# Kernel optimization log

Hardware: AMD Instinct MI355X
Metric: run time of the kernel (lower is better)

## Reference

```python
import jax, jax.numpy as jnp
import numpy as np

N = 100000      # nodes
E = 1600000     # edges (avg degree 16)
NF = 1          # node_feature_dim
EF = 1          # edge_feature_dim
H = 64          # hidden_dim
L = 5           # num_layers


def _linear_init(key, fan_in, fan_out):
    # torch nn.Linear default: U(-1/sqrt(fan_in), 1/sqrt(fan_in)) for W and b
    s = 1.0 / np.sqrt(fan_in)
    kw, kb = jax.random.split(key)
    w = jax.random.uniform(kw, (fan_in, fan_out), minval=-s, maxval=s, dtype=jnp.float32)
    b = jax.random.uniform(kb, (fan_out,), minval=-s, maxval=s, dtype=jnp.float32)
    return w, b


def setup_inputs() -> dict:
    key = jax.random.key(0)
    ks = jax.random.split(key, 8)
    x = jax.random.normal(ks[0], (N, NF), dtype=jnp.float32)
    edge_index = jax.random.randint(ks[1], (2, E), 0, N, dtype=jnp.int32)
    edge_attr = jax.random.uniform(ks[2], (E, EF), dtype=jnp.float32)

    emb_w, emb_b = _linear_init(ks[3], NF, H)
    fc_w, fc_b = _linear_init(ks[4], H, 1)

    msg_w1, msg_b1, msg_w2, msg_b2 = [], [], [], []
    upd_w1, upd_b1, upd_w2, upd_b2 = [], [], [], []
    lk = jax.random.split(ks[5], L)
    for l in range(L):
        k1, k2, k3, k4 = jax.random.split(lk[l], 4)
        w, b = _linear_init(k1, H + EF, H); msg_w1.append(w); msg_b1.append(b)
        w, b = _linear_init(k2, H, H);      msg_w2.append(w); msg_b2.append(b)
        w, b = _linear_init(k3, 2 * H, H);  upd_w1.append(w); upd_b1.append(b)
        w, b = _linear_init(k4, H, H);      upd_w2.append(w); upd_b2.append(b)

    stack = lambda xs: jnp.stack(xs, axis=0)
    return {
        "x": x, "edge_index": edge_index, "edge_attr": edge_attr,
        "emb_w": emb_w, "emb_b": emb_b,
        "msg_w1": stack(msg_w1), "msg_b1": stack(msg_b1),
        "msg_w2": stack(msg_w2), "msg_b2": stack(msg_b2),
        "upd_w1": stack(upd_w1), "upd_b1": stack(upd_b1),
        "upd_w2": stack(upd_w2), "upd_b2": stack(upd_b2),
        "fc_w": fc_w, "fc_b": fc_b,
    }


def reference(x, edge_index, edge_attr, emb_w, emb_b,
              msg_w1, msg_b1, msg_w2, msg_b2,
              upd_w1, upd_b1, upd_w2, upd_b2, fc_w, fc_b):
    src = edge_index[0]  # x_j (source)
    dst = edge_index[1]  # aggregation target i
    n = x.shape[0]

    h = x @ emb_w + emb_b  # [N, H]
    for l in range(msg_w1.shape[0]):
        # message: MLP(cat[x_j, edge_attr])
        m = jnp.concatenate([h[src], edge_attr], axis=1)  # [E, H+EF]
        m = jax.nn.relu(m @ msg_w1[l] + msg_b1[l]) @ msg_w2[l] + msg_b2[l]  # [E, H]
        # scatter-min aggregate; torch_scatter fills empty segments with 0
        aggr = jax.ops.segment_min(m, dst, num_segments=n)
        aggr = jnp.where(jnp.isfinite(aggr), aggr, jnp.zeros_like(aggr))
        # update: MLP(cat[x, aggr])
        u = jnp.concatenate([h, aggr], axis=1)  # [N, 2H]
        h = jax.nn.relu(u @ upd_w1[l] + upd_b1[l]) @ upd_w2[l] + upd_b2[l]
    return (h @ fc_w + fc_b).squeeze(-1)  # [N]
```

## Files before the change

### kernel.cpp

```cpp
#include <hip/hip_runtime.h>
#include <math.h>

#define N_NODES 100000
#define N_EDGES 1600000
#define HDIM 64
#define SCAN_T 1024
#define SCAN_CHUNK 98
#define NPB 128
#define LBLOCKS 782

__device__ __forceinline__ unsigned encMin(float f) {
  unsigned u = __float_as_uint(f);
  return (u & 0x80000000u) ? ~u : (u | 0x80000000u);
}
__device__ __forceinline__ float decMin(unsigned u) {
  unsigned b = (u & 0x80000000u) ? (u & 0x7FFFFFFFu) : ~u;
  return __uint_as_float(b);
}


__global__ __launch_bounds__(256) void k_zero_int(int* __restrict__ p, int n) {
  int i = blockIdx.x * 256 + threadIdx.x;
  if (i < n) p[i] = 0;
}

__global__ __launch_bounds__(256) void k_deg_count(const int* __restrict__ ei,
                                                   int* __restrict__ deg) {
  int e = blockIdx.x * 256 + threadIdx.x;
  if (e < N_EDGES) atomicAdd(&deg[ei[N_EDGES + e]], 1);
}

__global__ __launch_bounds__(SCAN_T) void k_rowptr(const int* __restrict__ deg,
                                                   int* __restrict__ row_ptr) {
  __shared__ int sums[SCAN_T];
  const int t = threadIdx.x;
  const int lo = t * SCAN_CHUNK;
  const int hi = min(lo + SCAN_CHUNK, N_NODES);
  int s = 0;
  for (int i = lo; i < hi; ++i) s += deg[i];
  sums[t] = s;
  __syncthreads();
  for (int off = 1; off < SCAN_T; off <<= 1) {
    int v = (t >= off) ? sums[t - off] : 0;
    __syncthreads();
    sums[t] += v;
    __syncthreads();
  }
  int run = (t == 0) ? 0 : sums[t - 1];
  for (int i = lo; i < hi; ++i) { row_ptr[i] = run; run += deg[i]; }
  if (t == SCAN_T - 1) row_ptr[N_NODES] = run;
}

__global__ __launch_bounds__(256) void k_scatter(
    const int* __restrict__ ei, const float* __restrict__ eattr,
    const int* __restrict__ row_ptr, int* __restrict__ cursor,
    int* __restrict__ s_src, float* __restrict__ s_ea, int* __restrict__ s_dl) {
  int e = blockIdx.x * 256 + threadIdx.x;
  if (e >= N_EDGES) return;
  int d = ei[N_EDGES + e];
  int pos = row_ptr[d] + atomicAdd(&cursor[d], 1);
  s_src[pos] = ei[e];
  s_ea[pos] = eattr[e];
  s_dl[pos] = d & (NPB - 1);
}


__global__ __launch_bounds__(256) void k_embed_z(
    const float* __restrict__ x, const float* __restrict__ emb_w,
    const float* __restrict__ emb_b,
    const float* __restrict__ w1, const float* __restrict__ b1,
    float* __restrict__ h, float* __restrict__ z) {
  __shared__ float hs[64][65];
  const int t = threadIdx.x;
  const int nl = t >> 2;
  const int l4 = t & 3;
  const int i = blockIdx.x * 64 + nl;
  const bool valid = (i < N_NODES);
  const int jbase = l4 * 16;
  const float xv = valid ? x[i] : 0.0f;

  float hv[16];
  #pragma unroll
  for (int jj = 0; jj < 16; ++jj) {
    int j = jbase + jj;
    hv[jj] = fmaf(xv, emb_w[j], emb_b[j]);
    hs[nl][j] = hv[jj];
  }
  if (valid) {
    #pragma unroll
    for (int q = 0; q < 4; ++q)
      reinterpret_cast<float4*>(h + (size_t)i * HDIM)[l4 * 4 + q] =
          make_float4(hv[4*q], hv[4*q+1], hv[4*q+2], hv[4*q+3]);
  }
  __syncthreads();

  float acc[16];
  #pragma unroll
  for (int jj = 0; jj < 16; ++jj) acc[jj] = b1[jbase + jj];
  #pragma unroll 8
  for (int k = 0; k < 64; ++k) {
    float hk = hs[nl][k];
    const float* wr = w1 + k * 64 + jbase;
    #pragma unroll
    for (int jj = 0; jj < 16; ++jj) acc[jj] = fmaf(hk, wr[jj], acc[jj]);
  }
  if (valid) {
    #pragma unroll
    for (int q = 0; q < 4; ++q)
      reinterpret_cast<float4*>(z + (size_t)i * HDIM)[l4 * 4 + q] =
          make_float4(acc[4*q], acc[4*q+1], acc[4*q+2], acc[4*q+3]);
  }
}

template <int LAST>
__global__ __launch_bounds__(256) void k_layer(
    const int* __restrict__ row_ptr,
    const int* __restrict__ s_src, const float* __restrict__ s_ea,
    const int* __restrict__ s_dl,
    const float* __restrict__ z_in,
    const float* __restrict__ w1b, const float* __restrict__ w2,
    const float* __restrict__ b2,
    const float* __restrict__ u1w, const float* __restrict__ u1b,
    const float* __restrict__ u2w, const float* __restrict__ u2b,
    const float* __restrict__ w1next, const float* __restrict__ b1next,
    const float* __restrict__ fcw, const float* __restrict__ fcb,
    float* __restrict__ h, float* __restrict__ z_out, float* __restrict__ out) {
  __shared__ float hid_s[4][8][68];
  __shared__ unsigned acc_u[NPB][65];
  __shared__ float ps[NPB][2];
  float* acc_f = (float*)acc_u;

  const int t = threadIdx.x;
  const int lane = t & 63;
  const int w = __builtin_amdgcn_readfirstlane(t >> 6);
  const int nbase = blockIdx.x * NPB;

  for (int i = t; i < NPB * 65; i += 256) ((unsigned*)acc_u)[i] = 0xFFFFFFFFu;
  __syncthreads();

  {
    const int eb0 = row_ptr[nbase];
    const int eb1 = row_ptr[min(nbase + NPB, N_NODES)];
    const int n = eb1 - eb0;
    const int we0 = eb0 + (n * w) / 4;
    const int we1 = eb0 + (n * (w + 1)) / 4;

    const int eL = lane >> 3;
    const int q  = lane & 7;
    const float4 w1bA = ((const float4*)w1b)[q];
    const float4 w1bB = ((const float4*)w1b)[8 + q];
    const float b2c = b2[lane];
    float w2c[64];
    #pragma unroll
    for (int k = 0; k < 64; ++k) w2c[k] = w2[k * 64 + lane];

    float run = INFINITY;
    int cur = -1;

    float4 ra, rb; float eaR = 0.0f;
    ra = make_float4(0.f,0.f,0.f,0.f); rb = ra;
    if (we0 + eL < we1) {
      const int src = s_src[we0 + eL];
      const float4* zr = (const float4*)(z_in + (size_t)src * HDIM);
      ra = zr[q]; rb = zr[8 + q];
      eaR = s_ea[we0 + eL];
    }

    for (int b = we0; b < we1; b += 8) {
      float4 na = make_float4(0.f,0.f,0.f,0.f), nb = na; float ean = 0.0f;
      if (b + 8 + eL < we1) {
        const int srcn = s_src[b + 8 + eL];
        const float4* zrn = (const float4*)(z_in + (size_t)srcn * HDIM);
        na = zrn[q]; nb = zrn[8 + q];
        ean = s_ea[b + 8 + eL];
      }
      if (b + eL < we1) {
        float4 h0, h1;
        h0.x = fmaxf(fmaf(eaR, w1bA.x, ra.x), 0.f);
        h0.y = fmaxf(fmaf(eaR, w1bA.y, ra.y), 0.f);
        h0.z = fmaxf(fmaf(eaR, w1bA.z, ra.z), 0.f);
        h0.w = fmaxf(fmaf(eaR, w1bA.w, ra.w), 0.f);
        h1.x = fmaxf(fmaf(eaR, w1bB.x, rb.x), 0.f);
        h1.y = fmaxf(fmaf(eaR, w1bB.y, rb.y), 0.f);
        h1.z = fmaxf(fmaf(eaR, w1bB.z, rb.z), 0.f);
        h1.w = fmaxf(fmaf(eaR, w1bB.w, rb.w), 0.f);
        *(float4*)&hid_s[w][eL][q * 4] = h0;
        *(float4*)&hid_s[w][eL][32 + q * 4] = h1;
      }
      #pragma unroll
      for (int e2 = 0; e2 < 8; ++e2) {
        if (b + e2 >= we1) break;
        float m0 = b2c, m1 = 0.f, m2 = 0.f, m3 = 0.f;
        #pragma unroll
        for (int k4 = 0; k4 < 16; ++k4) {
          float4 hq = *(const float4*)&hid_s[w][e2][k4 * 4];
          m0 = fmaf(hq.x, w2c[4*k4+0], m0);
          m1 = fmaf(hq.y, w2c[4*k4+1], m1);
          m2 = fmaf(hq.z, w2c[4*k4+2], m2);
          m3 = fmaf(hq.w, w2c[4*k4+3], m3);
        }
        float m = (m0 + m1) + (m2 + m3);
        const int dl = s_dl[b + e2];
        if (dl != cur) {
          if (cur >= 0) atomicMin(&acc_u[cur][lane], encMin(run));
          cur = dl; run = INFINITY;
        }
        run = fminf(run, m);
      }
      ra = na; rb = nb; eaR = ean;
    }
    if (cur >= 0) atomicMin(&acc_u[cur][lane], encMin(run));
  }
  __syncthreads();

  const int half = w & 1;
  const int pr = w >> 1;
  const int jb = half * 32;
  const int nl = pr * 64 + lane;
  const int node = nbase + nl;
  const bool valid = (node < N_NODES);
  const size_t off = (size_t)(valid ? node : 0) * HDIM;

  #pragma unroll
  for (int j = 0; j < 32; ++j) {
    float f = decMin(acc_u[nl][jb + j]);
    if (!isfinite(f)) f = 0.f;
    acc_f[nl * 65 + jb + j] = f;
  }
  __syncthreads();

  float acc[32];
  #pragma unroll
  for (int j = 0; j < 32; ++j) acc[j] = u1b[jb + j];
  {
    const float4* hr = reinterpret_cast<const float4*>(h + off);
    for (int k4 = 0; k4 < 16; ++k4) {
      float4 uv = hr[k4];
      const float* w0 = u1w + (4*k4+0) * 64 + jb;
      const float* w1 = u1w + (4*k4+1) * 64 + jb;
      const float* w2r = u1w + (4*k4+2) * 64 + jb;
      const float* w3 = u1w + (4*k4+3) * 64 + jb;
      #pragma unroll
      for (int j = 0; j < 32; ++j) acc[j] = fmaf(uv.x, w0[j], acc[j]);
      #pragma unroll
      for (int j = 0; j < 32; ++j) acc[j] = fmaf(uv.y, w1[j], acc[j]);
      #pragma unroll
      for (int j = 0; j < 32; ++j) acc[j] = fmaf(uv.z, w2r[j], acc[j]);
      #pragma unroll
      for (int j = 0; j < 32; ++j) acc[j] = fmaf(uv.w, w3[j], acc[j]);
    }
    #pragma unroll 4
    for (int k = 0; k < 64; ++k) {
      float uk = acc_f[nl * 65 + k];
      const float* wr = u1w + (64 + k) * 64 + jb;
      #pragma unroll
      for (int j = 0; j < 32; ++j) acc[j] = fmaf(uk, wr[j], acc[j]);
    }
  }
  __syncthreads();
  #pragma unroll
  for (int j = 0; j < 32; ++j) acc_f[nl * 65 + jb + j] = fmaxf(acc[j], 0.f);
  __syncthreads();

  float hn[32];
  #pragma unroll
  for (int j = 0; j < 32; ++j) hn[j] = u2b[jb + j];
  #pragma unroll 4
  for (int k = 0; k < 64; ++k) {
    float hk = acc_f[nl * 65 + k];
    const float* wr = u2w + k * 64 + jb;
    #pragma unroll
    for (int j = 0; j < 32; ++j) hn[j] = fmaf(hk, wr[j], hn[j]);
  }
  if (valid) {
    #pragma unroll
    for (int v = 0; v < 8; ++v)
      reinterpret_cast<float4*>(h + off)[half * 8 + v] =
          make_float4(hn[4*v], hn[4*v+1], hn[4*v+2], hn[4*v+3]);
  }

  if (LAST) {
    float s = 0.0f;
    #pragma unroll
    for (int j = 0; j < 32; ++j) s = fmaf(hn[j], fcw[jb + j], s);
    ps[nl][half] = s;
    __syncthreads();
    if (half == 0 && valid) out[node] = ps[nl][0] + ps[nl][1] + fcb[0];
  } else {
    __syncthreads();
    #pragma unroll
    for (int j = 0; j < 32; ++j) acc_f[nl * 65 + jb + j] = hn[j];
    __syncthreads();
    float zz[32];
    #pragma unroll
    for (int j = 0; j < 32; ++j) zz[j] = b1next[jb + j];
    #pragma unroll 4
    for (int k = 0; k < 64; ++k) {
      float hk = acc_f[nl * 65 + k];
      const float* wr = w1next + k * 64 + jb;
      #pragma unroll
      for (int j = 0; j < 32; ++j) zz[j] = fmaf(hk, wr[j], zz[j]);
    }
    if (valid) {
      #pragma unroll
      for (int v = 0; v < 8; ++v)
        reinterpret_cast<float4*>(z_out + off)[half * 8 + v] =
            make_float4(zz[4*v], zz[4*v+1], zz[4*v+2], zz[4*v+3]);
    }
  }
}

extern "C" void kernel_launch(void* const* d_in, const int* in_sizes, int n_in,
                              void* d_out, int out_size, void* d_ws, size_t ws_size,
                              hipStream_t stream) {
  const float* x      = (const float*)d_in[0];
  const int*   ei     = (const int*)d_in[1];
  const float* eattr  = (const float*)d_in[2];
  const float* emb_w  = (const float*)d_in[3];
  const float* emb_b  = (const float*)d_in[4];
  const float* msg_w1 = (const float*)d_in[5];
  const float* msg_b1 = (const float*)d_in[6];
  const float* msg_w2 = (const float*)d_in[7];
  const float* msg_b2 = (const float*)d_in[8];
  const float* upd_w1 = (const float*)d_in[9];
  const float* upd_b1 = (const float*)d_in[10];
  const float* upd_w2 = (const float*)d_in[11];
  const float* upd_b2 = (const float*)d_in[12];
  const float* fc_w   = (const float*)d_in[13];
  const float* fc_b   = (const float*)d_in[14];
  float* out = (float*)d_out;

  float* h     = (float*)d_ws;
  float* zA    = h + (size_t)N_NODES * HDIM;
  float* zB    = zA + (size_t)N_NODES * HDIM;
  float* s_ea  = zB + (size_t)N_NODES * HDIM;
  int*   s_src = (int*)(s_ea + N_EDGES);
  int*   s_dl  = s_src + N_EDGES;
  int*   row_ptr = s_dl + N_EDGES;
  int*   deg   = row_ptr + (N_NODES + 1);
  int*   cursor= deg + N_NODES;

  const int nodeBlocks64 = (N_NODES + 63) / 64;
  const int edgeBlocks = (N_EDGES + 255) / 256;

  k_zero_int<<<(2 * N_NODES + 255) / 256, 256, 0, stream>>>(deg, 2 * N_NODES);
  k_deg_count<<<edgeBlocks, 256, 0, stream>>>(ei, deg);
  k_rowptr<<<1, SCAN_T, 0, stream>>>(deg, row_ptr);
  k_scatter<<<edgeBlocks, 256, 0, stream>>>(ei, eattr, row_ptr, cursor,
                                            s_src, s_ea, s_dl);

  k_embed_z<<<nodeBlocks64, 256, 0, stream>>>(x, emb_w, emb_b, msg_w1, msg_b1, h, zA);

  float* zin = zA;
  float* zout = zB;
  for (int l = 0; l < 5; ++l) {
    const float* w1b = msg_w1 + l * 65 * 64 + 64 * 64;
    const float* w2  = msg_w2 + l * 64 * 64;
    const float* b2  = msg_b2 + l * 64;
    const float* u1w = upd_w1 + l * 128 * 64;
    const float* u1b = upd_b1 + l * 64;
    const float* u2w = upd_w2 + l * 64 * 64;
    const float* u2b = upd_b2 + l * 64;
    if (l < 4) {
      k_layer<0><<<LBLOCKS, 256, 0, stream>>>(
          row_ptr, s_src, s_ea, s_dl, zin,
          w1b, w2, b2, u1w, u1b, u2w, u2b,
          msg_w1 + (l + 1) * 65 * 64, msg_b1 + (l + 1) * 64,
          nullptr, nullptr,
          h, zout, nullptr);
      float* tmp = zin; zin = zout; zout = tmp;
    } else {
      k_layer<1><<<LBLOCKS, 256, 0, stream>>>(
          row_ptr, s_src, s_ea, s_dl, zin,
          w1b, w2, b2, u1w, u1b, u2w, u2b,
          nullptr, nullptr,
          fc_w, fc_b,
          h, nullptr, out);
    }
  }
}
```

Before: 2.560 ms.

## Restructure edge message MLP into batched 64-edge tiles with edge-per-lane matmul

Edge processing now works in 64-edge batches per wave pair. Each batch writes the hidden activations to shared memory, then each lane computes one edge's 32 output channels, with the w2 weights read as wave-uniform scalars instead of held as a 64-register column per lane. The per-node update MLP also drops to 64 nodes per block, with each wave computing 16 output columns, which doubles the block count. In exchange there are several block-wide barriers per batch, an extra shared-memory round trip for the message outputs, and the old prefetch of the next edge's gather is gone.

```diff
diff --git a/kernel.cpp b/kernel.cpp
--- a/kernel.cpp
+++ b/kernel.cpp
@@ -6,8 +6,9 @@
 #define HDIM 64
 #define SCAN_T 1024
 #define SCAN_CHUNK 98
-#define NPB 128
-#define LBLOCKS 782
+#define NPB 64
+#define LBLOCKS 1563
+#define BSTRIDE 66
 
 __device__ __forceinline__ unsigned encMin(float f) {
   unsigned u = __float_as_uint(f);
@@ -125,187 +126,204 @@
     const float* __restrict__ w1next, const float* __restrict__ b1next,
     const float* __restrict__ fcw, const float* __restrict__ fcb,
     float* __restrict__ h, float* __restrict__ z_out, float* __restrict__ out) {
-  __shared__ float hid_s[4][8][68];
+  __shared__ float buf[2][64][BSTRIDE];
   __shared__ unsigned acc_u[NPB][65];
-  __shared__ float ps[NPB][2];
+  __shared__ float ps[NPB][4];
   float* acc_f = (float*)acc_u;
 
   const int t = threadIdx.x;
   const int lane = t & 63;
   const int w = __builtin_amdgcn_readfirstlane(t >> 6);
+  const int pair = w >> 1;
+  const int wi = w & 1;
   const int nbase = blockIdx.x * NPB;
 
   for (int i = t; i < NPB * 65; i += 256) ((unsigned*)acc_u)[i] = 0xFFFFFFFFu;
-  __syncthreads();
-
-  {
-    const int eb0 = row_ptr[nbase];
-    const int eb1 = row_ptr[min(nbase + NPB, N_NODES)];
-    const int n = eb1 - eb0;
-    const int we0 = eb0 + (n * w) / 4;
-    const int we1 = eb0 + (n * (w + 1)) / 4;
-
-    const int eL = lane >> 3;
-    const int q  = lane & 7;
-    const float4 w1bA = ((const float4*)w1b)[q];
-    const float4 w1bB = ((const float4*)w1b)[8 + q];
-    const float b2c = b2[lane];
-    float w2c[64];
-    #pragma unroll
-    for (int k = 0; k < 64; ++k) w2c[k] = w2[k * 64 + lane];
-
-    float run = INFINITY;
-    int cur = -1;
-
-    float4 ra, rb; float eaR = 0.0f;
-    ra = make_float4(0.f,0.f,0.f,0.f); rb = ra;
-    if (we0 + eL < we1) {
-      const int src = s_src[we0 + eL];
-      const float4* zr = (const float4*)(z_in + (size_t)src * HDIM);
-      ra = zr[q]; rb = zr[8 + q];
-      eaR = s_ea[we0 + eL];
-    }
-
-    for (int b = we0; b < we1; b += 8) {
-      float4 na = make_float4(0.f,0.f,0.f,0.f), nb = na; float ean = 0.0f;
-      if (b + 8 + eL < we1) {
-        const int srcn = s_src[b + 8 + eL];
-        const float4* zrn = (const float4*)(z_in + (size_t)srcn * HDIM);
-        na = zrn[q]; nb = zrn[8 + q];
-        ean = s_ea[b + 8 + eL];
+
+  const int eb0 = row_ptr[nbase];
+  const int eb1 = row_ptr[min(nbase + NPB, N_NODES)];
+  const int n = eb1 - eb0;
+  const int emid = eb0 + (n >> 1);
+  const int p0 = pair ? emid : eb0;
+  const int p1 = pair ? eb1 : emid;
+  const int nbat = ((n - (n >> 1)) + 63) >> 6;
+
+  const int rq = lane >> 3;
+  const int q  = lane & 7;
+  const float4 w1bA = ((const float4*)w1b)[q];
+  const float4 w1bB = ((const float4*)w1b)[q + 8];
+  const int jb = wi * 32;
+
+  __syncthreads();
+
+  for (int bi = 0; bi < nbat; ++bi) {
+    const int base = p0 + (bi << 6);
+    const int cnt  = min(64, p1 - base);
+
+    if (cnt > 0) {
+      #pragma unroll
+      for (int i = 0; i < 4; ++i) {
+        const int row = wi * 32 + i * 8 + rq;
+        const int ed = base + row;
+        const bool v = (row < cnt);
+        const int src = v ? s_src[ed] : 0;
+        const float ea = v ? s_ea[ed] : 0.0f;
+        const float4* zr = (const float4*)(z_in + (size_t)src * HDIM);
+        float4 a = zr[q];
+        float4 b = zr[q + 8];
+        float2 h0, h1, h2, h3;
+        h0.x = fmaxf(fmaf(ea, w1bA.x, a.x), 0.f);
+        h0.y = fmaxf(fmaf(ea, w1bA.y, a.y), 0.f);
+        h1.x = fmaxf(fmaf(ea, w1bA.z, a.z), 0.f);
+        h1.y = fmaxf(fmaf(ea, w1bA.w, a.w), 0.f);
+        h2.x = fmaxf(fmaf(ea, w1bB.x, b.x), 0.f);
+        h2.y = fmaxf(fmaf(ea, w1bB.y, b.y), 0.f);
+        h3.x = fmaxf(fmaf(ea, w1bB.z, b.z), 0.f);
+        h3.y = fmaxf(fmaf(ea, w1bB.w, b.w), 0.f);
+        float* bp = &buf[pair][row][0];
+        *(float2*)&bp[q * 4]          = h0;
+        *(float2*)&bp[q * 4 + 2]      = h1;
+        *(float2*)&bp[32 + q * 4]     = h2;
+        *(float2*)&bp[32 + q * 4 + 2] = h3;
       }
-      if (b + eL < we1) {
-        float4 h0, h1;
-        h0.x = fmaxf(fmaf(eaR, w1bA.x, ra.x), 0.f);
-        h0.y = fmaxf(fmaf(eaR, w1bA.y, ra.y), 0.f);
-        h0.z = fmaxf(fmaf(eaR, w1bA.z, ra.z), 0.f);
-        h0.w = fmaxf(fmaf(eaR, w1bA.w, ra.w), 0.f);
-        h1.x = fmaxf(fmaf(eaR, w1bB.x, rb.x), 0.f);
-        h1.y = fmaxf(fmaf(eaR, w1bB.y, rb.y), 0.f);
-        h1.z = fmaxf(fmaf(eaR, w1bB.z, rb.z), 0.f);
-        h1.w = fmaxf(fmaf(eaR, w1bB.w, rb.w), 0.f);
-        *(float4*)&hid_s[w][eL][q * 4] = h0;
-        *(float4*)&hid_s[w][eL][32 + q * 4] = h1;
+    }
+    __syncthreads();
+
+    float m[32];
+    if (cnt > 0) {
+      #pragma unroll
+      for (int c = 0; c < 32; ++c) m[c] = b2[jb + c];
+      const float* bp = &buf[pair][lane][0];
+      #pragma unroll 4
+      for (int k2 = 0; k2 < 32; ++k2) {
+        float2 hq = *(const float2*)&bp[k2 * 2];
+        const float* wr0 = w2 + (2 * k2 + 0) * 64 + jb;
+        const float* wr1 = w2 + (2 * k2 + 1) * 64 + jb;
+        #pragma unroll
+        for (int c = 0; c < 32; ++c) m[c] = fmaf(hq.x, wr0[c], m[c]);
+        #pragma unroll
+        for (int c = 0; c < 32; ++c) m[c] = fmaf(hq.y, wr1[c], m[c]);
       }
-      #pragma unroll
-      for (int e2 = 0; e2 < 8; ++e2) {
-        if (b + e2 >= we1) break;
-        float m0 = b2c, m1 = 0.f, m2 = 0.f, m3 = 0.f;
-        #pragma unroll
-        for (int k4 = 0; k4 < 16; ++k4) {
-          float4 hq = *(const float4*)&hid_s[w][e2][k4 * 4];
-          m0 = fmaf(hq.x, w2c[4*k4+0], m0);
-          m1 = fmaf(hq.y, w2c[4*k4+1], m1);
-          m2 = fmaf(hq.z, w2c[4*k4+2], m2);
-          m3 = fmaf(hq.w, w2c[4*k4+3], m3);
-        }
-        float m = (m0 + m1) + (m2 + m3);
-        const int dl = s_dl[b + e2];
+    }
+    __syncthreads();
+
+    if (cnt > 0) {
+      float* bp = &buf[pair][lane][jb];
+      #pragma unroll
+      for (int c2 = 0; c2 < 16; ++c2)
+        *(float2*)&bp[c2 * 2] = make_float2(m[2*c2], m[2*c2+1]);
+    }
+    __syncthreads();
+
+    if (cnt > 0) {
+      const int e0 = wi * 32;
+      const int e1 = min(wi * 32 + 32, cnt);
+      float run = INFINITY;
+      int cur = -1;
+      for (int e = e0; e < e1; ++e) {
+        const int dl = s_dl[base + e];
         if (dl != cur) {
           if (cur >= 0) atomicMin(&acc_u[cur][lane], encMin(run));
           cur = dl; run = INFINITY;
         }
-        run = fminf(run, m);
+        run = fminf(run, buf[pair][e][lane]);
       }
-      ra = na; rb = nb; eaR = ean;
-    }
-    if (cur >= 0) atomicMin(&acc_u[cur][lane], encMin(run));
-  }
-  __syncthreads();
-
-  const int half = w & 1;
-  const int pr = w >> 1;
-  const int jb = half * 32;
-  const int nl = pr * 64 + lane;
-  const int node = nbase + nl;
+      if (cur >= 0) atomicMin(&acc_u[cur][lane], encMin(run));
+    }
+    __syncthreads();
+  }
+
+  const int jq = w * 16;
+  const int node = nbase + lane;
   const bool valid = (node < N_NODES);
   const size_t off = (size_t)(valid ? node : 0) * HDIM;
 
   #pragma unroll
-  for (int j = 0; j < 32; ++j) {
-    float f = decMin(acc_u[nl][jb + j]);
+  for (int j = 0; j < 16; ++j) {
+    float f = decMin(acc_u[lane][jq + j]);
     if (!isfinite(f)) f = 0.f;
-    acc_f[nl * 65 + jb + j] = f;
-  }
-  __syncthreads();
-
-  float acc[32];
-  #pragma unroll
-  for (int j = 0; j < 32; ++j) acc[j] = u1b[jb + j];
+    acc_f[lane * 65 + jq + j] = f;
+  }
+  __syncthreads();
+
+  float acc[16];
+  #pragma unroll
+  for (int j = 0; j < 16; ++j) acc[j] = u1b[jq + j];
   {
     const float4* hr = reinterpret_cast<const float4*>(h + off);
     for (int k4 = 0; k4 < 16; ++k4) {
       float4 uv = hr[k4];
-      const float* w0 = u1w + (4*k4+0) * 64 + jb;
-      const float* w1 = u1w + (4*k4+1) * 64 + jb;
-      const float* w2r = u1w + (4*k4+2) * 64 + jb;
-      const float* w3 = u1w + (4*k4+3) * 64 + jb;
-      #pragma unroll
-      for (int j = 0; j < 32; ++j) acc[j] = fmaf(uv.x, w0[j], acc[j]);
-      #pragma unroll
-      for (int j = 0; j < 32; ++j) acc[j] = fmaf(uv.y, w1[j], acc[j]);
-      #pragma unroll
-      for (int j = 0; j < 32; ++j) acc[j] = fmaf(uv.z, w2r[j], acc[j]);
-      #pragma unroll
-      for (int j = 0; j < 32; ++j) acc[j] = fmaf(uv.w, w3[j], acc[j]);
+      const float* w0 = u1w + (4*k4+0) * 64 + jq;
+      const float* w1 = u1w + (4*k4+1) * 64 + jq;
+      const float* w2r = u1w + (4*k4+2) * 64 + jq;
+      const float* w3 = u1w + (4*k4+3) * 64 + jq;
+      #pragma unroll
+      for (int j = 0; j < 16; ++j) acc[j] = fmaf(uv.x, w0[j], acc[j]);
+      #pragma unroll
+      for (int j = 0; j < 16; ++j) acc[j] = fmaf(uv.y, w1[j], acc[j]);
+      #pragma unroll
+      for (int j = 0; j < 16; ++j) acc[j] = fmaf(uv.z, w2r[j], acc[j]);
+      #pragma unroll
+      for (int j = 0; j < 16; ++j) acc[j] = fmaf(uv.w, w3[j], acc[j]);
     }
     #pragma unroll 4
     for (int k = 0; k < 64; ++k) {
-      float uk = acc_f[nl * 65 + k];
-      const float* wr = u1w + (64 + k) * 64 + jb;
-      #pragma unroll
-      for (int j = 0; j < 32; ++j) acc[j] = fmaf(uk, wr[j], acc[j]);
-    }
-  }
-  __syncthreads();
-  #pragma unroll
-  for (int j = 0; j < 32; ++j) acc_f[nl * 65 + jb + j] = fmaxf(acc[j], 0.f);
-  __syncthreads();
-
-  float hn[32];
-  #pragma unroll
-  for (int j = 0; j < 32; ++j) hn[j] = u2b[jb + j];
+      float uk = acc_f[lane * 65 + k];
+      const float* wr = u1w + (64 + k) * 64 + jq;
+      #pragma unroll
+      for (int j = 0; j < 16; ++j) acc[j] = fmaf(uk, wr[j], acc[j]);
+    }
+  }
+  __syncthreads();
+  #pragma unroll
+  for (int j = 0; j < 16; ++j) acc_f[lane * 65 + jq + j] = fmaxf(acc[j], 0.f);
+  __syncthreads();
+
+  float hn[16];
+  #pragma unroll
+  for (int j = 0; j < 16; ++j) hn[j] = u2b[jq + j];
   #pragma unroll 4
   for (int k = 0; k < 64; ++k) {
-    float hk = acc_f[nl * 65 + k];
-    const float* wr = u2w + k * 64 + jb;
-    #pragma unroll
-    for (int j = 0; j < 32; ++j) hn[j] = fmaf(hk, wr[j], hn[j]);
+    float hk = acc_f[lane * 65 + k];
+    const float* wr = u2w + k * 64 + jq;
+    #pragma unroll
+    for (int j = 0; j < 16; ++j) hn[j] = fmaf(hk, wr[j], hn[j]);
   }
   if (valid) {
     #pragma unroll
-    for (int v = 0; v < 8; ++v)
-      reinterpret_cast<float4*>(h + off)[half * 8 + v] =
-          make_float4(hn[4*v], hn[4*v+1], hn[4*v+2], hn[4*v+3]);
+    for (int v4 = 0; v4 < 4; ++v4)
+      reinterpret_cast<float4*>(h + off)[w * 4 + v4] =
+          make_float4(hn[4*v4], hn[4*v4+1], hn[4*v4+2], hn[4*v4+3]);
   }
 
   if (LAST) {
     float s = 0.0f;
     #pragma unroll
-    for (int j = 0; j < 32; ++j) s = fmaf(hn[j], fcw[jb + j], s);
-    ps[nl][half] = s;
-    __syncthreads();
-    if (half == 0 && valid) out[node] = ps[nl][0] + ps[nl][1] + fcb[0];
+    for (int j = 0; j < 16; ++j) s = fmaf(hn[j], fcw[jq + j], s);
+    ps[lane][w] = s;
+    __syncthreads();
+    if (w == 0 && valid)
+      out[node] = ps[lane][0] + ps[lane][1] + ps[lane][2] + ps[lane][3] + fcb[0];
   } else {
     __syncthreads();
     #pragma unroll
-    for (int j = 0; j < 32; ++j) acc_f[nl * 65 + jb + j] = hn[j];
-    __syncthreads();
-    float zz[32];
-    #pragma unroll
-    for (int j = 0; j < 32; ++j) zz[j] = b1next[jb + j];
+    for (int j = 0; j < 16; ++j) acc_f[lane * 65 + jq + j] = hn[j];
+    __syncthreads();
+    float zz[16];
+    #pragma unroll
+    for (int j = 0; j < 16; ++j) zz[j] = b1next[jq + j];
     #pragma unroll 4
     for (int k = 0; k < 64; ++k) {
-      float hk = acc_f[nl * 65 + k];
-      const float* wr = w1next + k * 64 + jb;
-      #pragma unroll
-      for (int j = 0; j < 32; ++j) zz[j] = fmaf(hk, wr[j], zz[j]);
+      float hk = acc_f[lane * 65 + k];
+      const float* wr = w1next + k * 64 + jq;
+      #pragma unroll
+      for (int j = 0; j < 16; ++j) zz[j] = fmaf(hk, wr[j], zz[j]);
     }
     if (valid) {
       #pragma unroll
-      for (int v = 0; v < 8; ++v)
-        reinterpret_cast<float4*>(z_out + off)[half * 8 + v] =
-            make_float4(zz[4*v], zz[4*v+1], zz[4*v+2], zz[4*v+3]);
+      for (int v4 = 0; v4 < 4; ++v4)
+        reinterpret_cast<float4*>(z_out + off)[w * 4 + v4] =
+            make_float4(zz[4*v4], zz[4*v4+1], zz[4*v4+2], zz[4*v4+3]);
     }
   }
 }
```

Measured after the change: 2.219 ms. -13.3%, faster.
